# Kernel optimization log

Hardware: AMD Instinct MI355X
Metric: run time of the kernel (lower is better)

Reference implementation:

```python
import jax, jax.numpy as jnp
import numpy as np


def _combine(left, right):
    # complex mult-add combine: (a_r, x_r) o (a_l, x_l) = (a_r*a_l, a_r*x_l + x_r)
    alr, ali, xlr, xli = left
    arr, ari, xrr, xri = right
    rar = arr * alr - ari * ali
    rai = arr * ali + ari * alr
    rxr = arr * xlr - ari * xli + xrr
    rxi = arr * xli + ari * xlr + xri
    return (rar, rai, rxr, rxi)


def setup_inputs() -> dict:
    key = jax.random.key(0)
    k1, k2, k3, k4 = jax.random.split(key, 4)
    B, L, D = 8, 4096, 256
    A_re = jax.random.uniform(k1, (B, L, D), dtype=jnp.float32)  # |a|<1-ish for stability
    A_im = jax.random.normal(k2, (B, L, D), dtype=jnp.float32) * 0.1
    X_re = jax.random.normal(k3, (B, L, D), dtype=jnp.float32)
    X_im = jax.random.normal(k4, (B, L, D), dtype=jnp.float32)
    return {"A_re": A_re, "A_im": A_im, "X_re": X_re, "X_im": X_im}


def reference(A_re, A_im, X_re, X_im):
    # Inclusive scan of y_t = a_t * y_{t-1} + x_t (complex), over time axis 1.
    _, _, yr, yi = jax.lax.associative_scan(_combine, (A_re, A_im, X_re, X_im), axis=1)
    # [B, L, D, 2] real/imag stacked (equivalent of torch.view_as_real of the complex output)
    return jnp.stack([yr, yi], axis=-1)
```

## Files before the change

kernel.cpp:

```cpp
#include <hip/hip_runtime.h>

#define BATCH 8
#define SEQ   4096
#define DIM   256

__global__ __launch_bounds__(DIM) void k_tile_agg(
    const float* __restrict__ Ar, const float* __restrict__ Ai,
    const float* __restrict__ Xr, const float* __restrict__ Xi,
    float4* __restrict__ agg, int NT, int T)
{
    int b = blockIdx.x / NT;
    int j = blockIdx.x - b * NT;
    int d = threadIdx.x;
    size_t base = ((size_t)b * SEQ + (size_t)j * T) * DIM + d;

    float ar = 1.f, ai = 0.f, xr = 0.f, xi = 0.f;
#pragma unroll 4
    for (int t = 0; t < T; ++t) {
        size_t idx = base + (size_t)t * DIM;
        float car = Ar[idx], cai = Ai[idx];
        float cxr = Xr[idx], cxi = Xi[idx];
        float nar = car * ar - cai * ai;
        float nai = car * ai + cai * ar;
        float nxr = car * xr - cai * xi + cxr;
        float nxi = car * xi + cai * xr + cxi;
        ar = nar; ai = nai; xr = nxr; xi = nxi;
    }
    agg[((size_t)b * NT + j) * DIM + d] = make_float4(ar, ai, xr, xi);
}

__global__ __launch_bounds__(DIM) void k_scan_agg(float4* __restrict__ agg, int NT)
{
    int gid = blockIdx.x * blockDim.x + threadIdx.x;
    int b = gid / DIM;
    int d = gid - b * DIM;

    float ar = 1.f, ai = 0.f, xr = 0.f, xi = 0.f;
    for (int j = 0; j < NT; ++j) {
        size_t o = ((size_t)b * NT + j) * DIM + d;
        float4 v = agg[o];
        agg[o] = make_float4(xr, xi, 0.f, 0.f);
        float nar = v.x * ar - v.y * ai;
        float nai = v.x * ai + v.y * ar;
        float nxr = v.x * xr - v.y * xi + v.z;
        float nxi = v.x * xi + v.y * xr + v.w;
        ar = nar; ai = nai; xr = nxr; xi = nxi;
    }
}

__global__ __launch_bounds__(DIM) void k_apply(
    const float* __restrict__ Ar, const float* __restrict__ Ai,
    const float* __restrict__ Xr, const float* __restrict__ Xi,
    const float4* __restrict__ agg, float2* __restrict__ out, int NT, int T)
{
    int b = blockIdx.x / NT;
    int j = blockIdx.x - b * NT;
    int d = threadIdx.x;

    float4 p = agg[((size_t)b * NT + j) * DIM + d];
    float yr = p.x, yi = p.y;

    size_t base = ((size_t)b * SEQ + (size_t)j * T) * DIM + d;
#pragma unroll 4
    for (int t = 0; t < T; ++t) {
        size_t idx = base + (size_t)t * DIM;
        float car = Ar[idx], cai = Ai[idx];
        float cxr = Xr[idx], cxi = Xi[idx];
        float nyr = car * yr - cai * yi + cxr;
        float nyi = car * yi + cai * yr + cxi;
        yr = nyr; yi = nyi;
        out[idx] = make_float2(yr, yi);
    }
}

extern "C" void kernel_launch(void* const* d_in, const int* in_sizes, int n_in,
                              void* d_out, int out_size, void* d_ws, size_t ws_size,
                              hipStream_t stream)
{
    const float* Ar = (const float*)d_in[0];
    const float* Ai = (const float*)d_in[1];
    const float* Xr = (const float*)d_in[2];
    const float* Xi = (const float*)d_in[3];
    float2* out = (float2*)d_out;
    float4* agg = (float4*)d_ws;

    int NT = 64;
    while (NT > 1 && (size_t)BATCH * NT * DIM * sizeof(float4) > ws_size) NT >>= 1;
    int T = SEQ / NT;

    dim3 block(DIM);
    dim3 grid1(BATCH * NT);
    k_tile_agg<<<grid1, block, 0, stream>>>(Ar, Ai, Xr, Xi, agg, NT, T);

    dim3 grid2((BATCH * DIM) / DIM);
    k_scan_agg<<<grid2, block, 0, stream>>>(agg, NT);

    k_apply<<<grid1, block, 0, stream>>>(Ar, Ai, Xr, Xi, agg, out, NT, T);
}
```

Measured before the change: 72.39 us.

## Vectorize scan kernels to float4 per lane and raise tile count

Each wave now handles a whole time tile, with every lane processing four consecutive channels through float4 loads and two float4 stores of interleaved output. The number of time tiles goes from 64 to 256, so the grid has more parallel work and each tile's serial recurrence is shorter. The intent is to cut the number of memory instructions and expose more concurrency on a bandwidth-bound scan. In exchange the serial aggregate scan runs four times as many steps, and the larger workspace needs more memory.

```diff
diff --git a/kernel.cpp b/kernel.cpp
--- a/kernel.cpp
+++ b/kernel.cpp
@@ -4,36 +4,56 @@
 #define SEQ   4096
 #define DIM   256
 
-__global__ __launch_bounds__(DIM) void k_tile_agg(
+
+__global__ __launch_bounds__(256) void k_tile_agg(
     const float* __restrict__ Ar, const float* __restrict__ Ai,
     const float* __restrict__ Xr, const float* __restrict__ Xi,
     float4* __restrict__ agg, int NT, int T)
 {
-    int b = blockIdx.x / NT;
-    int j = blockIdx.x - b * NT;
-    int d = threadIdx.x;
+    int wave = threadIdx.x >> 6;
+    int lane = threadIdx.x & 63;
+    int tile = blockIdx.x * 4 + wave;
+    int b = tile / NT;
+    int j = tile - b * NT;
+    int d = lane * 4;
+
     size_t base = ((size_t)b * SEQ + (size_t)j * T) * DIM + d;
 
-    float ar = 1.f, ai = 0.f, xr = 0.f, xi = 0.f;
+    float ar[4], ai[4], xr[4], xi[4];
+#pragma unroll
+    for (int k = 0; k < 4; ++k) { ar[k] = 1.f; ai[k] = 0.f; xr[k] = 0.f; xi[k] = 0.f; }
+
 #pragma unroll 4
     for (int t = 0; t < T; ++t) {
         size_t idx = base + (size_t)t * DIM;
-        float car = Ar[idx], cai = Ai[idx];
-        float cxr = Xr[idx], cxi = Xi[idx];
-        float nar = car * ar - cai * ai;
-        float nai = car * ai + cai * ar;
-        float nxr = car * xr - cai * xi + cxr;
-        float nxi = car * xi + cai * xr + cxi;
-        ar = nar; ai = nai; xr = nxr; xi = nxi;
+        float4 car = *(const float4*)(Ar + idx);
+        float4 cai = *(const float4*)(Ai + idx);
+        float4 cxr = *(const float4*)(Xr + idx);
+        float4 cxi = *(const float4*)(Xi + idx);
+        const float* pab = (const float*)&car;
+        const float* pai = (const float*)&cai;
+        const float* pxr = (const float*)&cxr;
+        const float* pxi = (const float*)&cxi;
+#pragma unroll
+        for (int k = 0; k < 4; ++k) {
+            float a_r = pab[k], a_i = pai[k], x_r = pxr[k], x_i = pxi[k];
+            float nar = a_r * ar[k] - a_i * ai[k];
+            float nai = a_r * ai[k] + a_i * ar[k];
+            float nxr = a_r * xr[k] - a_i * xi[k] + x_r;
+            float nxi = a_r * xi[k] + a_i * xr[k] + x_i;
+            ar[k] = nar; ai[k] = nai; xr[k] = nxr; xi[k] = nxi;
+        }
     }
-    agg[((size_t)b * NT + j) * DIM + d] = make_float4(ar, ai, xr, xi);
+    size_t o = ((size_t)b * NT + j) * DIM + d;
+#pragma unroll
+    for (int k = 0; k < 4; ++k)
+        agg[o + k] = make_float4(ar[k], ai[k], xr[k], xi[k]);
 }
 
 __global__ __launch_bounds__(DIM) void k_scan_agg(float4* __restrict__ agg, int NT)
 {
-    int gid = blockIdx.x * blockDim.x + threadIdx.x;
-    int b = gid / DIM;
-    int d = gid - b * DIM;
+    int b = blockIdx.x;
+    int d = threadIdx.x;
 
     float ar = 1.f, ai = 0.f, xr = 0.f, xi = 0.f;
     for (int j = 0; j < NT; ++j) {
@@ -48,28 +68,49 @@
     }
 }
 
-__global__ __launch_bounds__(DIM) void k_apply(
+__global__ __launch_bounds__(256) void k_apply(
     const float* __restrict__ Ar, const float* __restrict__ Ai,
     const float* __restrict__ Xr, const float* __restrict__ Xi,
-    const float4* __restrict__ agg, float2* __restrict__ out, int NT, int T)
+    const float4* __restrict__ agg, float* __restrict__ outf, int NT, int T)
 {
-    int b = blockIdx.x / NT;
-    int j = blockIdx.x - b * NT;
-    int d = threadIdx.x;
+    int wave = threadIdx.x >> 6;
+    int lane = threadIdx.x & 63;
+    int tile = blockIdx.x * 4 + wave;
+    int b = tile / NT;
+    int j = tile - b * NT;
+    int d = lane * 4;
 
-    float4 p = agg[((size_t)b * NT + j) * DIM + d];
-    float yr = p.x, yi = p.y;
+    float yr[4], yi[4];
+    size_t o = ((size_t)b * NT + j) * DIM + d;
+#pragma unroll
+    for (int k = 0; k < 4; ++k) {
+        float4 p = agg[o + k];
+        yr[k] = p.x; yi[k] = p.y;
+    }
 
     size_t base = ((size_t)b * SEQ + (size_t)j * T) * DIM + d;
 #pragma unroll 4
     for (int t = 0; t < T; ++t) {
         size_t idx = base + (size_t)t * DIM;
-        float car = Ar[idx], cai = Ai[idx];
-        float cxr = Xr[idx], cxi = Xi[idx];
-        float nyr = car * yr - cai * yi + cxr;
-        float nyi = car * yi + cai * yr + cxi;
-        yr = nyr; yi = nyi;
-        out[idx] = make_float2(yr, yi);
+        float4 car = *(const float4*)(Ar + idx);
+        float4 cai = *(const float4*)(Ai + idx);
+        float4 cxr = *(const float4*)(Xr + idx);
+        float4 cxi = *(const float4*)(Xi + idx);
+        const float* pab = (const float*)&car;
+        const float* pai = (const float*)&cai;
+        const float* pxr = (const float*)&cxr;
+        const float* pxi = (const float*)&cxi;
+#pragma unroll
+        for (int k = 0; k < 4; ++k) {
+            float nyr = pab[k] * yr[k] - pai[k] * yi[k] + pxr[k];
+            float nyi = pab[k] * yi[k] + pai[k] * yr[k] + pxi[k];
+            yr[k] = nyr; yi[k] = nyi;
+        }
+        float4 o1 = make_float4(yr[0], yi[0], yr[1], yi[1]);
+        float4 o2 = make_float4(yr[2], yi[2], yr[3], yi[3]);
+        float* po = outf + 2 * idx;
+        *(float4*)(po)     = o1;
+        *(float4*)(po + 4) = o2;
     }
 }
 
@@ -81,19 +122,17 @@
     const float* Ai = (const float*)d_in[1];
     const float* Xr = (const float*)d_in[2];
     const float* Xi = (const float*)d_in[3];
-    float2* out = (float2*)d_out;
+    float* outf = (float*)d_out;
     float4* agg = (float4*)d_ws;
 
-    int NT = 64;
-    while (NT > 1 && (size_t)BATCH * NT * DIM * sizeof(float4) > ws_size) NT >>= 1;
+    int NT = 256;
+    while (NT > 4 && (size_t)BATCH * NT * DIM * sizeof(float4) > ws_size) NT >>= 1;
     int T = SEQ / NT;
 
-    dim3 block(DIM);
-    dim3 grid1(BATCH * NT);
+    dim3 block(256);
+    dim3 grid1((BATCH * NT) / 4);
+
     k_tile_agg<<<grid1, block, 0, stream>>>(Ar, Ai, Xr, Xi, agg, NT, T);
-
-    dim3 grid2((BATCH * DIM) / DIM);
-    k_scan_agg<<<grid2, block, 0, stream>>>(agg, NT);
-
-    k_apply<<<grid1, block, 0, stream>>>(Ar, Ai, Xr, Xi, agg, out, NT, T);
+    k_scan_agg<<<BATCH, dim3(DIM), 0, stream>>>(agg, NT);
+    k_apply<<<grid1, block, 0, stream>>>(Ar, Ai, Xr, Xi, agg, outf, NT, T);
 }
```

Result: slower. 125.2 us (+72.9%).
